# Optimization experiments

Measured on AMD Instinct MI355X. Metric: run time of the kernel, lower is better.

The kernel has to match this reference:

```python
import jax, jax.numpy as jnp
import numpy as np

EMB = 256
VOCAB = 50000
STEPS = 100  # max extra decode iterations after the first (output rows = 101)
BN_EPS = 1e-5


def setup_inputs() -> dict:
    key = jax.random.key(0)
    ks = jax.random.split(key, 10)
    s = 0.05
    return {
        "board": jax.random.normal(ks[0], (19, 19), jnp.float32),
        "conv_w": jax.random.normal(ks[1], (1, 1, 3, 3), jnp.float32) * s,
        "conv_b": jnp.zeros((1,), jnp.float32),
        "bn_gamma": jnp.ones((1,), jnp.float32),
        "bn_beta": jnp.zeros((1,), jnp.float32),
        "p": jnp.ones((8,), jnp.float32),
        "W_lin": jax.random.normal(ks[2], (EMB, 361), jnp.float32) * s,
        "b_lin": jnp.zeros((EMB,), jnp.float32),
        "W_ih": jax.random.normal(ks[3], (4 * EMB, EMB), jnp.float32) * s,
        "b_ih": jnp.zeros((4 * EMB,), jnp.float32),
        "W_hh": jax.random.normal(ks[4], (4 * EMB, EMB), jnp.float32) * s,
        "b_hh": jnp.zeros((4 * EMB,), jnp.float32),
        "W_dec": jax.random.normal(ks[5], (VOCAB, EMB), jnp.float32) * s,
        "b_dec": jnp.zeros((VOCAB,), jnp.float32),
    }


def reference(board, conv_w, conv_b, bn_gamma, bn_beta, p,
              W_lin, b_lin, W_ih, b_ih, W_hh, b_hh, W_dec, b_dec):
    # --- shared conv + batchnorm (training-mode stats), all 8 "layers" share weights ---
    def conv_bn(x):  # x: [1,1,19,19]
        y = jax.lax.conv_general_dilated(x, conv_w, (1, 1), 'SAME') + conv_b.reshape(1, 1, 1, 1)
        mu = y.mean()
        var = jnp.mean((y - mu) ** 2)  # biased var over N,H,W (C=1)
        return bn_gamma[0] * (y - mu) * jax.lax.rsqrt(var + BN_EPS) + bn_beta[0]

    relu = jax.nn.relu
    x = board.reshape(1, 1, 19, 19)
    d1 = relu(p[0] * conv_bn(x))
    d2 = d1
    for i in (1, 3, 5):  # fixed structural unroll (residual pairs)
        d1 = relu(p[i] * conv_bn(d1))
        d1 = d2 = relu(p[i + 1] * conv_bn(d1) + d2)
    d1 = relu(conv_bn(d1))  # cnn_list[7], no scalar

    feat = W_lin @ d1.reshape(361) + b_lin  # [EMB]

    # --- LSTMCell (PyTorch gate order i,f,g,o) ---
    def cell(x_in, h, c):
        gates = W_ih @ x_in + b_ih + W_hh @ h + b_hh  # [4*EMB]
        i, f, g, o = jnp.split(gates, 4)
        c2 = jax.nn.sigmoid(f) * c + jax.nn.sigmoid(i) * jnp.tanh(g)
        h2 = jax.nn.sigmoid(o) * jnp.tanh(c2)
        return h2, c2

    zeros = jnp.zeros((EMB,), feat.dtype)
    h, c = cell(feat, zeros, zeros)
    logit0 = W_dec @ h + b_dec  # [VOCAB]

    # (original breaks early on argmax==3; max output rows = 101)
    def step(carry, _):
        h, c = carry
        h2, c2 = cell(h, h, c)
        return (h2, c2), W_dec @ h2 + b_dec

    _, logits = jax.lax.scan(step, (h, c), None, length=STEPS)  # [STEPS, VOCAB]
    out = jax.nn.relu(jnp.concatenate([logit0[None, :], logits], axis=0))  # [101, VOCAB]
    return out
```

## Files before the change

### kernel.cpp

```cpp
#include <hip/hip_runtime.h>
#include <math.h>

#define EMB 256
#define VOCAB 50000
#define TROWS 101
#define NLB 32
#define NW 4
#define NDECB 196
#define NTOT (NLB + NDECB)

__device__ __forceinline__ float sigf(float x) { return 1.0f / (1.0f + expf(-x)); }

__device__ __forceinline__ void pin4(float4& v) {
  asm volatile("" : "+v"(v.x), "+v"(v.y), "+v"(v.z), "+v"(v.w));
}

__global__ __launch_bounds__(384) void k_conv(
    const float* __restrict__ board, const float* __restrict__ conv_w,
    const float* __restrict__ conv_b, const float* __restrict__ bn_g,
    const float* __restrict__ bn_b, const float* __restrict__ p,
    float* __restrict__ d1g) {
  __shared__ float xa[361], xb[361];
  __shared__ float wred[6];
  __shared__ float mu_s, var_s;
  const int tid = threadIdx.x;
  const bool act = tid < 361;
  const int i = tid / 19, j = tid % 19;
  float cw[9];
#pragma unroll
  for (int q = 0; q < 9; q++) cw[q] = conv_w[q];
  const float cb = conv_b[0], gam = bn_g[0], bet = bn_b[0];
  if (act) xa[tid] = board[tid];
  __syncthreads();

  float d2 = 0.f;
  float* cur = xa;
  float* nxt = xb;
  for (int stage = 0; stage < 8; stage++) {
    float y = 0.f;
    if (act) {
#pragma unroll
      for (int di = 0; di < 3; di++) {
#pragma unroll
        for (int dj = 0; dj < 3; dj++) {
          int ii = i + di - 1, jj = j + dj - 1;
          float xv = (ii >= 0 && ii < 19 && jj >= 0 && jj < 19) ? cur[ii * 19 + jj] : 0.f;
          y += cw[di * 3 + dj] * xv;
        }
      }
      y += cb;
    }
    float s = act ? y : 0.f;
#pragma unroll
    for (int o = 32; o > 0; o >>= 1) s += __shfl_xor(s, o);
    if ((tid & 63) == 0) wred[tid >> 6] = s;
    __syncthreads();
    if (tid == 0) {
      float tt = 0.f;
      for (int q = 0; q < 6; q++) tt += wred[q];
      mu_s = tt / 361.f;
    }
    __syncthreads();
    const float mu = mu_s;
    float d = act ? (y - mu) : 0.f;
    s = d * d;
#pragma unroll
    for (int o = 32; o > 0; o >>= 1) s += __shfl_xor(s, o);
    if ((tid & 63) == 0) wred[tid >> 6] = s;
    __syncthreads();
    if (tid == 0) {
      float tt = 0.f;
      for (int q = 0; q < 6; q++) tt += wred[q];
      var_s = tt / 361.f;
    }
    __syncthreads();
    const float xn = gam * (y - mu) * (1.0f / sqrtf(var_s + 1e-5f)) + bet;

    float v;
    if (stage == 0) {
      v = fmaxf(p[0] * xn, 0.f);
      d2 = v;
    } else if (stage == 7) {
      v = fmaxf(xn, 0.f);
    } else if (stage & 1) {
      v = fmaxf(p[stage] * xn, 0.f);
    } else {
      v = fmaxf(p[stage] * xn + d2, 0.f);
      d2 = v;
    }
    if (act) nxt[tid] = v;
    __syncthreads();
    float* tmp = cur; cur = nxt; nxt = tmp;
  }
  if (act) d1g[tid] = cur[tid];
}

__global__ __launch_bounds__(256) void k_feat(
    const float* __restrict__ W_lin, const float* __restrict__ b_lin,
    const float* __restrict__ d1g, float* __restrict__ feat) {
  const int wid = threadIdx.x >> 6, lane = threadIdx.x & 63;
  const int rbase = blockIdx.x * 16 + wid * 4;
  for (int rr = 0; rr < 4; rr++) {
    const int r = rbase + rr;
    const float* wrow = W_lin + r * 361;
    float s = 0.f;
    for (int k = lane; k < 361; k += 64) s += wrow[k] * d1g[k];
#pragma unroll
    for (int o = 32; o > 0; o >>= 1) s += __shfl_xor(s, o);
    if (lane == 0) feat[r] = s + b_lin[r];
  }
}

__global__ __launch_bounds__(512)
__attribute__((amdgpu_waves_per_eu(2, 2)))
void k_net(
    const float* __restrict__ W_ih, const float* __restrict__ b_ih,
    const float* __restrict__ W_hh, const float* __restrict__ b_hh,
    const float* __restrict__ feat, const float* __restrict__ W_dec,
    const float* __restrict__ b_dec, unsigned long long* hcomm,
    unsigned long long* xtab, unsigned* hflag, unsigned* hdec,
    float* __restrict__ out) {
  __shared__ float h_lds[EMB];
  __shared__ float gbuf[2][EMB];
  __shared__ float pbuf[2][EMB];
  __shared__ int sxcd[NLB];
  const int tid = threadIdx.x;

  if (blockIdx.x >= NLB) {
    const int db = blockIdx.x - NLB;
    const int w = tid >> 6, lane = tid & 63;
    const int sh = w & 1;
    const int rr = (w >> 1) * 64 + lane;
    const int v = db * 256 + rr;
    const int rv = v < VOCAB ? v : VOCAB - 1;
    float4 w4[32];
    {
      const float4* wr = (const float4*)(W_dec + rv * EMB + sh * 128);
#pragma unroll
      for (int q = 0; q < 32; q++) { w4[q] = wr[q]; pin4(w4[q]); }
    }
    const float bd = b_dec[rv];

    for (int t = 0; t < TROWS; t++) {
      if (w == 0) {
        const unsigned want = (unsigned)(t + 1);
        while (1) {
          const unsigned f0 = __hip_atomic_load(&hflag[t * 4 + 0], __ATOMIC_RELAXED, __HIP_MEMORY_SCOPE_AGENT);
          const unsigned f1 = __hip_atomic_load(&hflag[t * 4 + 1], __ATOMIC_RELAXED, __HIP_MEMORY_SCOPE_AGENT);
          const unsigned f2 = __hip_atomic_load(&hflag[t * 4 + 2], __ATOMIC_RELAXED, __HIP_MEMORY_SCOPE_AGENT);
          const unsigned f3 = __hip_atomic_load(&hflag[t * 4 + 3], __ATOMIC_RELAXED, __HIP_MEMORY_SCOPE_AGENT);
          if (((f0 ^ want) | (f1 ^ want) | (f2 ^ want) | (f3 ^ want)) == 0u) break;
          __builtin_amdgcn_s_sleep(2);
        }
      }
      __syncthreads();

      const float p0 = __uint_as_float(__hip_atomic_load(
          &hdec[t * EMB + sh * 128 + lane], __ATOMIC_RELAXED, __HIP_MEMORY_SCOPE_AGENT));
      const float p1 = __uint_as_float(__hip_atomic_load(
          &hdec[t * EMB + sh * 128 + 64 + lane], __ATOMIC_RELAXED, __HIP_MEMORY_SCOPE_AGENT));

      float a0 = 0.f, a1 = 0.f, a2 = 0.f, a3 = 0.f;
#pragma unroll
      for (int k = 0; k < 32; k++) {
        const float4 wv = w4[k];
        const int kk = 4 * k;
        const float s0 = __uint_as_float(__builtin_amdgcn_readlane(
            __float_as_uint(kk + 0 < 64 ? p0 : p1), (kk + 0) & 63));
        const float s1 = __uint_as_float(__builtin_amdgcn_readlane(
            __float_as_uint(kk + 1 < 64 ? p0 : p1), (kk + 1) & 63));
        const float s2 = __uint_as_float(__builtin_amdgcn_readlane(
            __float_as_uint(kk + 2 < 64 ? p0 : p1), (kk + 2) & 63));
        const float s3 = __uint_as_float(__builtin_amdgcn_readlane(
            __float_as_uint(kk + 3 < 64 ? p0 : p1), (kk + 3) & 63));
        a0 = fmaf(s0, wv.x, a0);
        a1 = fmaf(s1, wv.y, a1);
        a2 = fmaf(s2, wv.z, a2);
        a3 = fmaf(s3, wv.w, a3);
      }
      const float part = (a0 + a1) + (a2 + a3);
      if (sh) pbuf[t & 1][rr] = part;
      __syncthreads();
      if (!sh && v < VOCAB) {
        out[t * VOCAB + v] = fmaxf(part + pbuf[t & 1][rr] + bd, 0.f);
      }
    }
    return;
  }

  if (tid == 0) {
    unsigned xcc = __builtin_amdgcn_s_getreg(63508) & 7u;
    __hip_atomic_store(&xtab[blockIdx.x],
                       0xE1EC000000000000ULL | (unsigned long long)xcc,
                       __ATOMIC_RELAXED, __HIP_MEMORY_SCOPE_AGENT);
  }
  if (tid < NLB) {
    const unsigned long long* slot = &xtab[tid];
    unsigned long long u;
    while (1) {
      u = __hip_atomic_load(slot, __ATOMIC_RELAXED, __HIP_MEMORY_SCOPE_AGENT);
      if ((unsigned)(u >> 32) == 0xE1EC0000u) break;
      __builtin_amdgcn_s_sleep(2);
    }
    sxcd[tid] = (int)((unsigned)u & 7u);
  }
  __syncthreads();
  int target = -1;
  for (int x = 0; x < 8; x++) {
    int n = 0;
    for (int b = 0; b < NLB; b++) n += (sxcd[b] == x);
    if (n >= NW) { target = x; break; }
  }
  int rank = -1, seen = 0;
  for (int b = 0; b < NLB; b++) {
    if (sxcd[b] == target) {
      if (b == (int)blockIdx.x) rank = seen;
      seen++;
    }
  }
  if (rank < 0 || rank >= NW) return;
  const int g = rank;

  const int w = tid >> 6, lane = tid & 63;
  const int half = w & 1;
  const int gate = w >> 1;
  const int rloc = gate * 64 + lane;
  const int R = gate * 256 + g * 64 + lane;
  const float bsum = b_ih[R] + b_hh[R];

  float4 w4[32];
  {
    const float4* wih = (const float4*)(W_ih + R * EMB + half * 128);
#pragma unroll
    for (int q = 0; q < 32; q++) { w4[q] = wih[q]; pin4(w4[q]); }
  }
  if (tid < EMB) h_lds[tid] = feat[tid];
  float c = 0.f;
  __syncthreads();

  for (int t = 0; t <= 100; t++) {
    const float hv0 = h_lds[half * 128 + lane];
    const float hv1 = h_lds[half * 128 + 64 + lane];

    float a0 = (half == 0) ? bsum : 0.f, a1 = 0.f, a2 = 0.f, a3 = 0.f;
#pragma unroll
    for (int k = 0; k < 32; k++) {
      const float4 wv = w4[k];
      const int kk = 4 * k;
      const float s0 = __uint_as_float(__builtin_amdgcn_readlane(
          __float_as_uint(kk + 0 < 64 ? hv0 : hv1), (kk + 0) & 63));
      const float s1 = __uint_as_float(__builtin_amdgcn_readlane(
          __float_as_uint(kk + 1 < 64 ? hv0 : hv1), (kk + 1) & 63));
      const float s2 = __uint_as_float(__builtin_amdgcn_readlane(
          __float_as_uint(kk + 2 < 64 ? hv0 : hv1), (kk + 2) & 63));
      const float s3 = __uint_as_float(__builtin_amdgcn_readlane(
          __float_as_uint(kk + 3 < 64 ? hv0 : hv1), (kk + 3) & 63));
      a0 = fmaf(s0, wv.x, a0);
      a1 = fmaf(s1, wv.y, a1);
      a2 = fmaf(s2, wv.z, a2);
      a3 = fmaf(s3, wv.w, a3);
    }
    gbuf[half][rloc] = (a0 + a1) + (a2 + a3);
    __syncthreads();

    if (tid < 64) {
      const float gi = gbuf[0][tid]       + gbuf[1][tid];
      const float gf = gbuf[0][64 + tid]  + gbuf[1][64 + tid];
      const float gg = gbuf[0][128 + tid] + gbuf[1][128 + tid];
      const float go = gbuf[0][192 + tid] + gbuf[1][192 + tid];
      c = sigf(gf) * c + sigf(gi) * tanhf(gg);
      const float h = sigf(go) * tanhf(c);
      const int j = g * 64 + tid;
      h_lds[j] = h;
      __hip_atomic_store(&hdec[t * EMB + j], __float_as_uint(h),
                         __ATOMIC_RELAXED, __HIP_MEMORY_SCOPE_AGENT);
      if (t < 100) {
        unsigned long long pkt =
            ((unsigned long long)(unsigned)(t + 1) << 32) | (unsigned long long)__float_as_uint(h);
        __hip_atomic_store(&hcomm[(t & 1) * EMB + j], pkt,
                           __ATOMIC_RELAXED, __HIP_MEMORY_SCOPE_AGENT);
      }
      if (tid == 0) {
        __hip_atomic_store(&hflag[t * 4 + g], (unsigned)(t + 1),
                           __ATOMIC_RELEASE, __HIP_MEMORY_SCOPE_AGENT);
      }
    }
    if (t < 100) {
      if (tid < EMB && (tid < g * 64 || tid >= g * 64 + 64)) {
        const unsigned long long* slot = &hcomm[(t & 1) * EMB + tid];
        unsigned long long u;
        while (1) {
          u = __hip_atomic_load(slot, __ATOMIC_RELAXED, __HIP_MEMORY_SCOPE_AGENT);
          if ((unsigned)(u >> 32) == (unsigned)(t + 1)) break;
        }
        h_lds[tid] = __uint_as_float((unsigned)u);
      }
      __syncthreads();
    }
    if (t == 0) {
      const float4* whh = (const float4*)(W_hh + R * EMB + half * 128);
#pragma unroll
      for (int q = 0; q < 32; q++) {
        float4 a = whh[q];
        w4[q].x += a.x; w4[q].y += a.y; w4[q].z += a.z; w4[q].w += a.w;
        pin4(w4[q]);
      }
    }
  }
}

extern "C" void kernel_launch(void* const* d_in, const int* in_sizes, int n_in,
                              void* d_out, int out_size, void* d_ws, size_t ws_size,
                              hipStream_t stream) {
  const float* board  = (const float*)d_in[0];
  const float* conv_w = (const float*)d_in[1];
  const float* conv_b = (const float*)d_in[2];
  const float* bn_g   = (const float*)d_in[3];
  const float* bn_b   = (const float*)d_in[4];
  const float* p      = (const float*)d_in[5];
  const float* W_lin  = (const float*)d_in[6];
  const float* b_lin  = (const float*)d_in[7];
  const float* W_ih   = (const float*)d_in[8];
  const float* b_ih   = (const float*)d_in[9];
  const float* W_hh   = (const float*)d_in[10];
  const float* b_hh   = (const float*)d_in[11];
  const float* W_dec  = (const float*)d_in[12];
  const float* b_dec  = (const float*)d_in[13];

  float* wsf = (float*)d_ws;
  float* feat = wsf;
  float* d1g  = wsf + 256;
  unsigned long long* hcomm = (unsigned long long*)(wsf + 640);
  unsigned long long* xtab  = hcomm + 512;
  unsigned* hflag = (unsigned*)(xtab + 32);
  unsigned* hdec  = hflag + 512;

  k_conv<<<1, 384, 0, stream>>>(board, conv_w, conv_b, bn_g, bn_b, p, d1g);
  k_feat<<<16, 256, 0, stream>>>(W_lin, b_lin, d1g, feat);
  k_net<<<NTOT, 512, 0, stream>>>(W_ih, b_ih, W_hh, b_hh, feat, W_dec, b_dec,
                                  hcomm, xtab, hflag, hdec, (float*)d_out);
}
```

Measured before the change: 370.9 us.

## Add fast sc0 polling channel for LSTM h exchange and defer decoder publish

Adds a second h exchange buffer written and polled with inline-asm global_store/load dwordx2 using the sc0 cache bit, checked three times before falling back to the agent-scope atomic slot. This targets lower latency on the cross-block recurrent handoff, which is the serial critical path. It also moves the hdec store and the hflag release for decoder blocks to after the h exchange, so the LSTM blocks publish to their peers first. The risk is coherence: sc0 loads may hit stale cache lines on some paths, and the code then relies on the atomic fallback. Decoder blocks also see h slightly later.

```diff
diff --git a/kernel.cpp b/kernel.cpp
--- a/kernel.cpp
+++ b/kernel.cpp
@@ -13,6 +13,16 @@
 
 __device__ __forceinline__ void pin4(float4& v) {
   asm volatile("" : "+v"(v.x), "+v"(v.y), "+v"(v.z), "+v"(v.w));
+}
+
+__device__ __forceinline__ void fast_store_u64(unsigned long long* p, unsigned long long v) {
+  asm volatile("global_store_dwordx2 %0, %1, off sc0" :: "v"(p), "v"(v) : "memory");
+}
+__device__ __forceinline__ unsigned long long fast_load_u64(const unsigned long long* p) {
+  unsigned long long r;
+  asm volatile("global_load_dwordx2 %0, %1, off sc0\n\ts_waitcnt vmcnt(0)"
+               : "=&v"(r) : "v"(p) : "memory");
+  return r;
 }
 
 __global__ __launch_bounds__(384) void k_conv(
@@ -119,7 +129,7 @@
     const float* __restrict__ feat, const float* __restrict__ W_dec,
     const float* __restrict__ b_dec, unsigned long long* hcomm,
     unsigned long long* xtab, unsigned* hflag, unsigned* hdec,
-    float* __restrict__ out) {
+    unsigned long long* hfast, float* __restrict__ out) {
   __shared__ float h_lds[EMB];
   __shared__ float gbuf[2][EMB];
   __shared__ float pbuf[2][EMB];
@@ -236,6 +246,7 @@
   }
   if (tid < EMB) h_lds[tid] = feat[tid];
   float c = 0.f;
+  float hmine = 0.f;
   __syncthreads();
 
   for (int t = 0; t <= 100; t++) {
@@ -270,32 +281,51 @@
       const float go = gbuf[0][192 + tid] + gbuf[1][192 + tid];
       c = sigf(gf) * c + sigf(gi) * tanhf(gg);
       const float h = sigf(go) * tanhf(c);
+      hmine = h;
       const int j = g * 64 + tid;
       h_lds[j] = h;
-      __hip_atomic_store(&hdec[t * EMB + j], __float_as_uint(h),
-                         __ATOMIC_RELAXED, __HIP_MEMORY_SCOPE_AGENT);
       if (t < 100) {
-        unsigned long long pkt =
+        const unsigned long long pkt =
             ((unsigned long long)(unsigned)(t + 1) << 32) | (unsigned long long)__float_as_uint(h);
+        fast_store_u64(&hfast[(t & 1) * EMB + j], pkt);
         __hip_atomic_store(&hcomm[(t & 1) * EMB + j], pkt,
                            __ATOMIC_RELAXED, __HIP_MEMORY_SCOPE_AGENT);
-      }
-      if (tid == 0) {
-        __hip_atomic_store(&hflag[t * 4 + g], (unsigned)(t + 1),
-                           __ATOMIC_RELEASE, __HIP_MEMORY_SCOPE_AGENT);
+      } else {
+        __hip_atomic_store(&hdec[t * EMB + j], __float_as_uint(h),
+                           __ATOMIC_RELAXED, __HIP_MEMORY_SCOPE_AGENT);
+        if (tid == 0) {
+          __hip_atomic_store(&hflag[t * 4 + g], (unsigned)(t + 1),
+                             __ATOMIC_RELEASE, __HIP_MEMORY_SCOPE_AGENT);
+        }
       }
     }
     if (t < 100) {
       if (tid < EMB && (tid < g * 64 || tid >= g * 64 + 64)) {
+        const unsigned want = (unsigned)(t + 1);
+        const unsigned long long* fsl = &hfast[(t & 1) * EMB + tid];
         const unsigned long long* slot = &hcomm[(t & 1) * EMB + tid];
         unsigned long long u;
         while (1) {
+          u = fast_load_u64(fsl);
+          if ((unsigned)(u >> 32) == want) break;
+          u = fast_load_u64(fsl);
+          if ((unsigned)(u >> 32) == want) break;
+          u = fast_load_u64(fsl);
+          if ((unsigned)(u >> 32) == want) break;
           u = __hip_atomic_load(slot, __ATOMIC_RELAXED, __HIP_MEMORY_SCOPE_AGENT);
-          if ((unsigned)(u >> 32) == (unsigned)(t + 1)) break;
+          if ((unsigned)(u >> 32) == want) break;
         }
         h_lds[tid] = __uint_as_float((unsigned)u);
       }
       __syncthreads();
+      if (tid < 64) {
+        __hip_atomic_store(&hdec[t * EMB + g * 64 + tid], __float_as_uint(hmine),
+                           __ATOMIC_RELAXED, __HIP_MEMORY_SCOPE_AGENT);
+        if (tid == 0) {
+          __hip_atomic_store(&hflag[t * 4 + g], (unsigned)(t + 1),
+                             __ATOMIC_RELEASE, __HIP_MEMORY_SCOPE_AGENT);
+        }
+      }
     }
     if (t == 0) {
       const float4* whh = (const float4*)(W_hh + R * EMB + half * 128);
@@ -334,9 +364,10 @@
   unsigned long long* xtab  = hcomm + 512;
   unsigned* hflag = (unsigned*)(xtab + 32);
   unsigned* hdec  = hflag + 512;
+  unsigned long long* hfast = (unsigned long long*)(hdec + TROWS * EMB + 96);
 
   k_conv<<<1, 384, 0, stream>>>(board, conv_w, conv_b, bn_g, bn_b, p, d1g);
   k_feat<<<16, 256, 0, stream>>>(W_lin, b_lin, d1g, feat);
   k_net<<<NTOT, 512, 0, stream>>>(W_ih, b_ih, W_hh, b_hh, feat, W_dec, b_dec,
-                                  hcomm, xtab, hflag, hdec, (float*)d_out);
-}
+                                  hcomm, xtab, hflag, hdec, hfast, (float*)d_out);
+}
```

Result: slower. 380.4 us (+2.6%).
